# Kernel optimization log

Measured on AMD Instinct MI355X. Metric: run time of the kernel, lower is better.

Reference implementation:

```python
import jax, jax.numpy as jnp
import numpy as np
import math

EPS = 1e-8      # module eps for log/clamp
BN_EPS = 1e-5   # torch BatchNorm1d default eps


def _bn(h, g, b, m, v):
    # eval-mode BatchNorm1d over channel dim of (B, C, P)
    scale = g / jnp.sqrt(v + BN_EPS)
    return (h - m[None, :, None]) * scale[None, :, None] + b[None, :, None]


def _conv(h, W, b):
    # Conv1d with kernel_size=1 == per-point channel mixing
    return jnp.einsum('oc,bcp->bop', W, h) + b[None, :, None]


def _pairwise_lv_fts(xi, xj, eps=EPS):
    # ParT pairwise Lorentz-vector features, num_outputs=4: (lnkt, lnz, lndelta, lnm2)
    def ptrapphi(p):
        px, py, pz, e = p[:, 0], p[:, 1], p[:, 2], p[:, 3]
        pt = jnp.sqrt(px * px + py * py)
        rap = 0.5 * jnp.log1p(2.0 * pz / jnp.maximum(e - pz, 1e-20))
        phi = jnp.arctan2(py, px)
        return pt, rap, phi

    pti, rapi, phii = ptrapphi(xi)
    ptj, rapj, phij = ptrapphi(xj)
    dphi = jnp.mod(phii - phij + math.pi, 2.0 * math.pi) - math.pi
    delta = jnp.sqrt((rapi - rapj) ** 2 + dphi ** 2)
    lndelta = jnp.log(jnp.maximum(delta, eps))
    ptmin = jnp.minimum(pti, ptj)
    lnkt = jnp.log(jnp.maximum(ptmin * delta, eps))
    lnz = jnp.log(jnp.maximum(ptmin / jnp.maximum(pti + ptj, eps), eps))
    xs = xi + xj
    m2 = jnp.maximum(xs[:, 3] ** 2 - xs[:, 0] ** 2 - xs[:, 1] ** 2 - xs[:, 2] ** 2, eps)
    lnm2 = jnp.log(m2)
    return jnp.stack([lnkt, lnz, lndelta, lnm2], axis=1)  # (B, 4, P)


def setup_inputs():
    key = jax.random.key(0)
    ks = jax.random.split(key, 8)
    B, S = 64, 128
    dims = [64, 64, 64]
    # physically valid 4-vectors: E = sqrt(|p|^2 + m^2), m = 0.1
    p3 = jax.random.normal(ks[0], (B, 3, S), dtype=jnp.float32) * 10.0
    e = jnp.sqrt(jnp.sum(p3 * p3, axis=1, keepdims=True) + 0.01)
    x = jnp.concatenate([p3, e], axis=1)  # (B, 4, S): px, py, pz, E

    def bn_p(k, c):
        k1, k2 = jax.random.split(k)
        return (jnp.ones(c), jnp.zeros(c),
                jax.random.normal(k1, (c,)) * 0.1,
                jax.random.uniform(k2, (c,)) * 0.5 + 0.5)

    inp = {'x': x}
    g, b, m, v = bn_p(ks[1], 4)
    inp.update({'bn0_g': g, 'bn0_b': b, 'bn0_m': m, 'bn0_v': v})
    in_c = 4
    for li, d in enumerate(dims, start=1):
        kw, kb, kbn = jax.random.split(ks[1 + li], 3)
        inp['W%d' % li] = jax.random.normal(kw, (d, in_c)) * (1.0 / np.sqrt(in_c).astype(np.float32))
        inp['b%d' % li] = jax.random.normal(kb, (d,)) * 0.01
        g, b, m, v = bn_p(kbn, d)
        inp['bn%d_g' % li] = g; inp['bn%d_b' % li] = b
        inp['bn%d_m' % li] = m; inp['bn%d_v' % li] = v
        in_c = d
    return inp


def reference(x, bn0_g, bn0_b, bn0_m, bn0_v,
              W1, b1, bn1_g, bn1_b, bn1_m, bn1_v,
              W2, b2, bn2_g, bn2_b, bn2_m, bn2_v,
              W3, b3, bn3_g, bn3_b, bn3_m, bn3_v):
    B, _, S = x.shape
    # symmetric path: lower-triangle pairs incl. diagonal (remove_self_pair=False)
    i, j = np.tril_indices(S, 0)
    xi = x[:, :, i]                      # (B, 4, P) gather
    xj = x[:, :, j]
    fts = _pairwise_lv_fts(xi, xj)       # (B, 4, P)
    h = _bn(fts, bn0_g, bn0_b, bn0_m, bn0_v)
    h = jax.nn.gelu(_bn(_conv(h, W1, b1), bn1_g, bn1_b, bn1_m, bn1_v), approximate=False)
    h = jax.nn.gelu(_bn(_conv(h, W2, b2), bn2_g, bn2_b, bn2_m, bn2_v), approximate=False)
    h = _bn(_conv(h, W3, b3), bn3_g, bn3_b, bn3_m, bn3_v)  # pre-activation output
    out_dim = h.shape[1]
    # scatter back into symmetric (B, out_dim, S, S)
    y = jnp.zeros((B, out_dim, S, S), h.dtype)
    y = y.at[:, :, i, j].set(h)
    y = y.at[:, :, j, i].set(h)
    return y
```

## Files before the change

### kernel.cpp

```cpp
#include <hip/hip_runtime.h>
#include <math.h>

#define S_TOK 128
#define PS_O 257

#define SWZ(row, byteoff) ((((row) * 128) + (byteoff)) ^ (((row) & 7) << 4))

#define OFF_A1 0
#define OFF_C1 256
#define OFF_C2 320
#define OFF_C3 384
#define OFF_BF 448

using bf16x8 = __attribute__((ext_vector_type(8))) __bf16;
using f32x4  = __attribute__((ext_vector_type(4))) float;

__device__ __forceinline__ unsigned short f2bf(float v) {
    unsigned u = __builtin_bit_cast(unsigned, v);
    u += 0x7fffu + ((u >> 16) & 1u);
    return (unsigned short)(u >> 16);
}

__device__ __forceinline__ float gelu_fast(float v) {
    float v2 = v * v;
    float z  = v * fmaf(0.044715f, v2, 1.0f);
    float u  = z * 2.3022082f;
    float e;
    asm("v_exp_f32 %0, %1" : "=v"(e) : "v"(u));
    float d = e + 1.0f;
    float r;
    asm("v_rcp_f32 %0, %1" : "=v"(r) : "v"(d));
    return fmaf(-v, r, v);
}

__global__ void fold_weights_kernel(
    const float* __restrict__ bn0g, const float* __restrict__ bn0b,
    const float* __restrict__ bn0m, const float* __restrict__ bn0v,
    const float* __restrict__ W1,  const float* __restrict__ b1,
    const float* __restrict__ bn1g, const float* __restrict__ bn1b,
    const float* __restrict__ bn1m, const float* __restrict__ bn1v,
    const float* __restrict__ W2,  const float* __restrict__ b2,
    const float* __restrict__ bn2g, const float* __restrict__ bn2b,
    const float* __restrict__ bn2m, const float* __restrict__ bn2v,
    const float* __restrict__ W3,  const float* __restrict__ b3,
    const float* __restrict__ bn3g, const float* __restrict__ bn3b,
    const float* __restrict__ bn3m, const float* __restrict__ bn3v,
    float* __restrict__ ws)
{
    int o = threadIdx.x;
    if (o >= 64) return;
    float s0[4], t0[4];
    #pragma unroll
    for (int c = 0; c < 4; ++c) {
        float s = bn0g[c] / sqrtf(bn0v[c] + 1e-5f);
        s0[c] = s;
        t0[c] = bn0b[c] - bn0m[c] * s;
    }
    float s1 = bn1g[o] / sqrtf(bn1v[o] + 1e-5f);
    float acc = b1[o] - bn1m[o];
    #pragma unroll
    for (int c = 0; c < 4; ++c) {
        float w = W1[o*4 + c];
        ws[OFF_A1 + o*4 + c] = s1 * w * s0[c];
        acc += w * t0[c];
    }
    ws[OFF_C1 + o] = s1 * acc + bn1b[o];

    unsigned short* wsbf = (unsigned short*)(ws + OFF_BF);
    unsigned short* A2bf = wsbf;
    unsigned short* A3bf = wsbf + 4096;

    float s2 = bn2g[o] / sqrtf(bn2v[o] + 1e-5f);
    for (int c = 0; c < 64; ++c) A2bf[o*64 + c] = f2bf(W2[o*64 + c] * s2);
    ws[OFF_C2 + o] = (b2[o] - bn2m[o]) * s2 + bn2b[o];

    float s3 = bn3g[o] / sqrtf(bn3v[o] + 1e-5f);
    for (int c = 0; c < 64; ++c) A3bf[o*64 + c] = f2bf(W3[o*64 + c] * s3);
    ws[OFF_C3 + o] = (b3[o] - bn3m[o]) * s3 + bn3b[o];
}

__global__ __launch_bounds__(256, 4) void pair_mlp_mfma(
    const float* __restrict__ x, const float* __restrict__ ws,
    float* __restrict__ y)
{
    __shared__ __align__(16) unsigned char Abuf[32768];

    const int t = blockIdx.x;
    const int b = blockIdx.y;
    int I = (int)((sqrtf(8.0f * (float)t + 1.0f) - 1.0f) * 0.5f);
    while ((I + 1) * (I + 2) / 2 <= t) ++I;
    while (I * (I + 1) / 2 > t) --I;
    const int J = t - I * (I + 1) / 2;

    const int tid  = threadIdx.x;
    const int lane = tid & 63;
    const int wv   = tid >> 6;
    const int lcol = lane & 15;
    const int lgrp = lane >> 4;

    const int li = tid >> 4;
    const int lj = tid & 15;
    const int i = I * 16 + li;
    const int j = J * 16 + lj;

    const float* xb = x + (size_t)b * 4 * S_TOK;
    const float pxi = xb[0*S_TOK + i], pyi = xb[1*S_TOK + i];
    const float pzi = xb[2*S_TOK + i], ei  = xb[3*S_TOK + i];
    const float pxj = xb[0*S_TOK + j], pyj = xb[1*S_TOK + j];
    const float pzj = xb[2*S_TOK + j], ej  = xb[3*S_TOK + j];

    const float pti = sqrtf(pxi*pxi + pyi*pyi);
    const float ptj = sqrtf(pxj*pxj + pyj*pyj);
    const float rapi = 0.5f * log1pf(2.0f * pzi / fmaxf(ei - pzi, 1e-20f));
    const float rapj = 0.5f * log1pf(2.0f * pzj / fmaxf(ej - pzj, 1e-20f));
    const float phii = atan2f(pyi, pxi);
    const float phij = atan2f(pyj, pxj);

    const float PI_F    = 3.14159265358979323846f;
    const float TWOPI_F = 6.28318530717958647692f;
    float dx   = phii - phij + PI_F;
    float dphi = dx - TWOPI_F * floorf(dx * (1.0f / TWOPI_F)) - PI_F;
    float drap = rapi - rapj;
    float delta = sqrtf(drap*drap + dphi*dphi);
    float lndelta = logf(fmaxf(delta, 1e-8f));
    float ptmin = fminf(pti, ptj);
    float f0 = logf(fmaxf(ptmin * delta, 1e-8f));
    float f1 = logf(fmaxf(ptmin / fmaxf(pti + ptj, 1e-8f), 1e-8f));
    float f2 = lndelta;
    float sx = pxi + pxj, sy = pyi + pyj, sz = pzi + pzj, se = ei + ej;
    float f3 = logf(fmaxf(se*se - sx*sx - sy*sy - sz*sz, 1e-8f));

    const float* A1 = ws + OFF_A1;
    const float* C1 = ws + OFF_C1;
    #pragma unroll
    for (int oc = 0; oc < 8; ++oc) {
        unsigned pk[4];
        #pragma unroll
        for (int q = 0; q < 4; ++q) {
            const int o0 = oc*8 + 2*q;
            float z0 = C1[o0]   + A1[o0*4+0]*f0 + A1[o0*4+1]*f1
                                + A1[o0*4+2]*f2 + A1[o0*4+3]*f3;
            float z1 = C1[o0+1] + A1[(o0+1)*4+0]*f0 + A1[(o0+1)*4+1]*f1
                                + A1[(o0+1)*4+2]*f2 + A1[(o0+1)*4+3]*f3;
            z0 = gelu_fast(z0);
            z1 = gelu_fast(z1);
            pk[q] = (unsigned)f2bf(z0) | ((unsigned)f2bf(z1) << 16);
        }
        uint4 v; v.x = pk[0]; v.y = pk[1]; v.z = pk[2]; v.w = pk[3];
        *reinterpret_cast<uint4*>(Abuf + SWZ(tid, oc*16)) = v;
    }
    __syncthreads();

    const unsigned short* A2bf = (const unsigned short*)(ws + OFF_BF);
    const unsigned short* A3bf = A2bf + 4096;
    const float* C2 = ws + OFF_C2;
    const float* C3 = ws + OFF_C3;

    f32x4 acc2[4][4];
    #pragma unroll
    for (int mt = 0; mt < 4; ++mt)
        #pragma unroll
        for (int nt = 0; nt < 4; ++nt)
            acc2[mt][nt] = f32x4{0.f, 0.f, 0.f, 0.f};
    {
        bf16x8 wf[4][2];
        #pragma unroll
        for (int nt = 0; nt < 4; ++nt)
            #pragma unroll
            for (int kt = 0; kt < 2; ++kt)
                wf[nt][kt] = *reinterpret_cast<const bf16x8*>(
                    A2bf + (nt*16 + lcol)*64 + kt*32 + lgrp*8);
        #pragma unroll
        for (int kt = 0; kt < 2; ++kt) {
            bf16x8 af[4];
            #pragma unroll
            for (int mt = 0; mt < 4; ++mt)
                af[mt] = *reinterpret_cast<const bf16x8*>(
                    Abuf + SWZ(wv*64 + mt*16 + lcol, kt*64 + lgrp*16));
            #pragma unroll
            for (int mt = 0; mt < 4; ++mt)
                #pragma unroll
                for (int nt = 0; nt < 4; ++nt)
                    acc2[mt][nt] = __builtin_amdgcn_mfma_f32_16x16x32_bf16(
                        af[mt], wf[nt][kt], acc2[mt][nt], 0, 0, 0);
        }
    }
    __syncthreads();

    #pragma unroll
    for (int nt = 0; nt < 4; ++nt) {
        const float bias = C2[nt*16 + lcol];
        #pragma unroll
        for (int mt = 0; mt < 4; ++mt)
            #pragma unroll
            for (int r = 0; r < 4; ++r) {
                float z = acc2[mt][nt][r] + bias;
                *reinterpret_cast<unsigned short*>(
                    Abuf + SWZ(wv*64 + mt*16 + 4*lgrp + r, (nt*16 + lcol)*2))
                    = f2bf(gelu_fast(z));
            }
    }
    __syncthreads();

    f32x4 acc3[4][4];
    #pragma unroll
    for (int mt = 0; mt < 4; ++mt)
        #pragma unroll
        for (int nt = 0; nt < 4; ++nt)
            acc3[mt][nt] = f32x4{0.f, 0.f, 0.f, 0.f};
    {
        bf16x8 wf[4][2];
        #pragma unroll
        for (int nt = 0; nt < 4; ++nt)
            #pragma unroll
            for (int kt = 0; kt < 2; ++kt)
                wf[nt][kt] = *reinterpret_cast<const bf16x8*>(
                    A3bf + (nt*16 + lcol)*64 + kt*32 + lgrp*8);
        #pragma unroll
        for (int kt = 0; kt < 2; ++kt) {
            bf16x8 af[4];
            #pragma unroll
            for (int mt = 0; mt < 4; ++mt)
                af[mt] = *reinterpret_cast<const bf16x8*>(
                    Abuf + SWZ(wv*64 + mt*16 + lcol, kt*64 + lgrp*16));
            #pragma unroll
            for (int mt = 0; mt < 4; ++mt)
                #pragma unroll
                for (int nt = 0; nt < 4; ++nt)
                    acc3[mt][nt] = __builtin_amdgcn_mfma_f32_16x16x32_bf16(
                        af[mt], wf[nt][kt], acc3[mt][nt], 0, 0, 0);
        }
    }

    const size_t ybase = (size_t)b * 64 * (S_TOK * S_TOK);
    const bool diag = (I == J);

    if (diag) {
        #pragma unroll
        for (int nt = 0; nt < 4; ++nt) {
            const float bias3 = C3[nt*16 + lcol];
            #pragma unroll
            for (int mt = 0; mt < 4; ++mt) {
                f32x4 v = acc3[mt][nt] + bias3;
                *reinterpret_cast<f32x4*>(
                    &y[ybase + (size_t)(nt*16 + lcol)*(S_TOK*S_TOK)
                             + (16*I + 4*wv + mt)*S_TOK + 16*J + 4*lgrp]) = v;
            }
        }
    } else {
        float* Obuf = reinterpret_cast<float*>(Abuf);
        const int jd = tid & 15;
        const int g2 = (tid >> 4) & 3;
        __syncthreads();

        for (int nt = 0; nt < 4; ++nt) {
            const float bias3 = C3[nt*16 + lcol];
            #pragma unroll
            for (int mt = 0; mt < 4; ++mt) {
                f32x4 v = acc3[mt][nt] + bias3;
                *reinterpret_cast<f32x4*>(
                    &y[ybase + (size_t)(nt*16 + lcol)*(S_TOK*S_TOK)
                             + (16*I + 4*wv + mt)*S_TOK + 16*J + 4*lgrp]) = v;
                const int il = 4*wv + mt;
                #pragma unroll
                for (int r = 0; r < 4; ++r) {
                    const int jl = 4*lgrp + r;
                    Obuf[lcol*PS_O + il*16 + ((jl + il) & 15)] = v[r];
                }
            }
            __syncthreads();
            #pragma unroll
            for (int k = 0; k < 16; ++k) {
                const int ol = 4*(k & 3) + wv;
                const int o  = nt*16 + ol;
                const int il = 4*(k >> 2) + g2;
                const float vmir = Obuf[ol*PS_O + jd*16 + ((il + jd) & 15)];
                y[ybase + (size_t)o*(S_TOK*S_TOK) + (16*J + il)*S_TOK + 16*I + jd] = vmir;
            }
            __syncthreads();
        }
    }
}

extern "C" void kernel_launch(void* const* d_in, const int* in_sizes, int n_in,
                              void* d_out, int out_size, void* d_ws, size_t ws_size,
                              hipStream_t stream) {
    const float* x    = (const float*)d_in[0];
    const float* bn0g = (const float*)d_in[1];
    const float* bn0b = (const float*)d_in[2];
    const float* bn0m = (const float*)d_in[3];
    const float* bn0v = (const float*)d_in[4];
    const float* W1   = (const float*)d_in[5];
    const float* b1   = (const float*)d_in[6];
    const float* bn1g = (const float*)d_in[7];
    const float* bn1b = (const float*)d_in[8];
    const float* bn1m = (const float*)d_in[9];
    const float* bn1v = (const float*)d_in[10];
    const float* W2   = (const float*)d_in[11];
    const float* b2   = (const float*)d_in[12];
    const float* bn2g = (const float*)d_in[13];
    const float* bn2b = (const float*)d_in[14];
    const float* bn2m = (const float*)d_in[15];
    const float* bn2v = (const float*)d_in[16];
    const float* W3   = (const float*)d_in[17];
    const float* b3   = (const float*)d_in[18];
    const float* bn3g = (const float*)d_in[19];
    const float* bn3b = (const float*)d_in[20];
    const float* bn3m = (const float*)d_in[21];
    const float* bn3v = (const float*)d_in[22];

    float* ws = (float*)d_ws;
    float* y  = (float*)d_out;

    fold_weights_kernel<<<1, 64, 0, stream>>>(
        bn0g, bn0b, bn0m, bn0v, W1, b1, bn1g, bn1b, bn1m, bn1v,
        W2, b2, bn2g, bn2b, bn2m, bn2v, W3, b3, bn3g, bn3b, bn3m, bn3v, ws);

    dim3 grid(36, 64);
    pair_mlp_mfma<<<grid, 256, 0, stream>>>(x, ws, y);
}
```

Before: 76.01 us.

## Stage mirrored output as bf16 in LDS, two channel tiles per barrier

```diff
diff --git a/kernel.cpp b/kernel.cpp
--- a/kernel.cpp
+++ b/kernel.cpp
@@ -2,9 +2,12 @@
 #include <math.h>
 
 #define S_TOK 128
-#define PS_O 257
 
 #define SWZ(row, byteoff) ((((row) * 128) + (byteoff)) ^ (((row) & 7) << 4))
+
+#define OB_ROW   20
+#define OB_PLANE 340
+#define OB_CHUNK 5440
 
 #define OFF_A1 0
 #define OFF_C1 256
@@ -19,6 +22,12 @@
     unsigned u = __builtin_bit_cast(unsigned, v);
     u += 0x7fffu + ((u >> 16) & 1u);
     return (unsigned short)(u >> 16);
+}
+
+__device__ __forceinline__ unsigned cvt_pk_bf16(float lo, float hi) {
+    unsigned pk;
+    asm("v_cvt_pk_bf16_f32 %0, %1, %2" : "=v"(pk) : "v"(lo), "v"(hi));
+    return pk;
 }
 
 __device__ __forceinline__ float gelu_fast(float v) {
@@ -142,9 +151,7 @@
                                 + A1[o0*4+2]*f2 + A1[o0*4+3]*f3;
             float z1 = C1[o0+1] + A1[(o0+1)*4+0]*f0 + A1[(o0+1)*4+1]*f1
                                 + A1[(o0+1)*4+2]*f2 + A1[(o0+1)*4+3]*f3;
-            z0 = gelu_fast(z0);
-            z1 = gelu_fast(z1);
-            pk[q] = (unsigned)f2bf(z0) | ((unsigned)f2bf(z1) << 16);
+            pk[q] = cvt_pk_bf16(gelu_fast(z0), gelu_fast(z1));
         }
         uint4 v; v.x = pk[0]; v.y = pk[1]; v.z = pk[2]; v.w = pk[3];
         *reinterpret_cast<uint4*>(Abuf + SWZ(tid, oc*16)) = v;
@@ -194,10 +201,11 @@
         for (int mt = 0; mt < 4; ++mt)
             #pragma unroll
             for (int r = 0; r < 4; ++r) {
-                float z = acc2[mt][nt][r] + bias;
+                float z = gelu_fast(acc2[mt][nt][r] + bias);
+                unsigned pk = cvt_pk_bf16(z, z);
                 *reinterpret_cast<unsigned short*>(
                     Abuf + SWZ(wv*64 + mt*16 + 4*lgrp + r, (nt*16 + lcol)*2))
-                    = f2bf(gelu_fast(z));
+                    = (unsigned short)pk;
             }
     }
     __syncthreads();
@@ -248,34 +256,46 @@
             }
         }
     } else {
-        float* Obuf = reinterpret_cast<float*>(Abuf);
+        unsigned short* ObufU = reinterpret_cast<unsigned short*>(Abuf);
         const int jd = tid & 15;
         const int g2 = (tid >> 4) & 3;
         __syncthreads();
 
-        for (int nt = 0; nt < 4; ++nt) {
-            const float bias3 = C3[nt*16 + lcol];
-            #pragma unroll
-            for (int mt = 0; mt < 4; ++mt) {
-                f32x4 v = acc3[mt][nt] + bias3;
-                *reinterpret_cast<f32x4*>(
-                    &y[ybase + (size_t)(nt*16 + lcol)*(S_TOK*S_TOK)
-                             + (16*I + 4*wv + mt)*S_TOK + 16*J + 4*lgrp]) = v;
-                const int il = 4*wv + mt;
+        for (int np = 0; np < 2; ++np) {
+            #pragma unroll
+            for (int sub = 0; sub < 2; ++sub) {
+                const int nt = 2*np + sub;
+                const float bias3 = C3[nt*16 + lcol];
                 #pragma unroll
-                for (int r = 0; r < 4; ++r) {
-                    const int jl = 4*lgrp + r;
-                    Obuf[lcol*PS_O + il*16 + ((jl + il) & 15)] = v[r];
+                for (int mt = 0; mt < 4; ++mt) {
+                    f32x4 v = acc3[mt][nt] + bias3;
+                    *reinterpret_cast<f32x4*>(
+                        &y[ybase + (size_t)(nt*16 + lcol)*(S_TOK*S_TOK)
+                                 + (16*I + 4*wv + mt)*S_TOK + 16*J + 4*lgrp]) = v;
+                    const int il = 4*wv + mt;
+                    const int s  = (4*(lgrp + il)) & 15;
+                    uint2 pkv;
+                    pkv.x = cvt_pk_bf16(v[0], v[1]);
+                    pkv.y = cvt_pk_bf16(v[2], v[3]);
+                    *reinterpret_cast<uint2*>(
+                        ObufU + sub*OB_CHUNK + lcol*OB_PLANE + il*OB_ROW + s) = pkv;
                 }
             }
             __syncthreads();
             #pragma unroll
-            for (int k = 0; k < 16; ++k) {
-                const int ol = 4*(k & 3) + wv;
-                const int o  = nt*16 + ol;
-                const int il = 4*(k >> 2) + g2;
-                const float vmir = Obuf[ol*PS_O + jd*16 + ((il + jd) & 15)];
-                y[ybase + (size_t)o*(S_TOK*S_TOK) + (16*J + il)*S_TOK + 16*I + jd] = vmir;
+            for (int sub = 0; sub < 2; ++sub) {
+                const int nt = 2*np + sub;
+                #pragma unroll
+                for (int k = 0; k < 16; ++k) {
+                    const int ol  = 4*(k & 3) + wv;
+                    const int o   = nt*16 + ol;
+                    const int ilr = 4*(k >> 2) + g2;
+                    const int col = (ilr + 4*jd) & 15;
+                    unsigned short u = ObufU[sub*OB_CHUNK + ol*OB_PLANE + jd*OB_ROW + col];
+                    float f = __builtin_bit_cast(float, ((unsigned)u) << 16);
+                    y[ybase + (size_t)o*(S_TOK*S_TOK)
+                            + (16*J + ilr)*S_TOK + 16*I + jd] = f;
+                }
             }
             __syncthreads();
         }
```

Measured after the change: 82.81 us. 8.9% more time.
